# Optimization experiments

Measured on AMD Instinct MI355X. Metric: run time of the kernel, lower is better.

The kernel has to match this reference:

```python
import jax, jax.numpy as jnp
import numpy as np

N, E, SEQ, IN, HID, OUT = 2048, 65536, 5, 32, 64, 16
EPS = 1e-5


def setup_inputs() -> dict:
    ks = jax.random.split(jax.random.key(0), 16)
    def w(k, shape):
        return jax.random.normal(k, shape, jnp.float32) / np.float32(np.sqrt(shape[0]))
    z = lambda n: jnp.zeros((n,), jnp.float32)
    return dict(
        x=jax.random.normal(ks[0], (SEQ, N, IN), jnp.float32),
        edge_weight=jax.random.uniform(ks[1], (E,), jnp.float32),
        Wcz=w(ks[2], (IN, HID)), bcz=z(HID), Wlz=w(ks[3], (2 * HID, HID)), blz=z(HID),
        Wcr=w(ks[4], (IN, HID)), bcr=z(HID), Wlr=w(ks[5], (2 * HID, HID)), blr=z(HID),
        Wch=w(ks[6], (IN, HID)), bch=z(HID), Wlh=w(ks[7], (2 * HID, HID)), blh=z(HID),
        Wred=w(ks[8], (SEQ * HID, HID)), bred=z(HID),
        Wc1=w(ks[9], (HID, HID)), bc1=z(HID), Wc2=w(ks[10], (HID, HID)), bc2=z(HID),
        g1=jnp.ones((HID,), jnp.float32), be1=z(HID),
        g2=jnp.ones((HID,), jnp.float32), be2=z(HID),
        Wout=w(ks[11], (HID, OUT)), bout=z(OUT),
        Wi1=w(ks[12], (2 * HID, HID)), bi1=z(HID),
        Wi2=w(ks[13], (HID, 1)), bi2=z(1),
        edge_index=jax.random.randint(ks[14], (2, E), 0, N),
    )


def _layer_norm(h, g, b):
    mu = jnp.mean(h, -1, keepdims=True)
    var = jnp.mean((h - mu) ** 2, -1, keepdims=True)
    return (h - mu) * jax.lax.rsqrt(var + EPS) * g + b


def _forward(x, edge_weight, Wcz, bcz, Wlz, blz, Wcr, bcr, Wlr, blr,
             Wch, bch, Wlh, blh, Wred, bred, Wc1, bc1, Wc2, bc2,
             g1, be1, g2, be2, Wout, bout, Wi1, bi1, Wi2, bi2, edge_index):
    src, dst = edge_index[0], edge_index[1]
    # GCN symmetric normalization with self-loops (weight 1.0); shared by all convs.
    deg = jax.ops.segment_sum(edge_weight, dst, num_segments=N) + 1.0
    dinv = jax.lax.rsqrt(deg)
    norm = dinv[src] * edge_weight * dinv[dst]  # [E]
    dself = dinv * dinv                          # [N] self-loop coefficient

    def gcn(h, W, b):
        hw = h @ W
        agg = jax.ops.segment_sum(norm[:, None] * hw[src], dst, num_segments=N)
        return agg + dself[:, None] * hw + b

    # TGCN per timestep. The original passes no hidden state, so H resets to 0
    # each call: H_t = (1 - Z) * tanh(candidate); reset gate R is multiplied by
    # H=0 and has no effect (its params get zero gradient, matching torch).
    hs = []
    for t in range(SEQ):  # SEQ=5, fixed small loop
        Zg = jax.nn.sigmoid(gcn(x[t], Wcz, bcz) @ Wlz[:HID] + blz)
        Ht = jnp.tanh(gcn(x[t], Wch, bch) @ Wlh[:HID] + blh)
        hs.append((1.0 - Zg) * Ht)
    h = jnp.stack(hs, axis=1).reshape(N, SEQ * HID)
    h = h @ Wred + bred
    emb = h  # intermediate embeddings for the interaction predictor
    h = gcn(h, Wc1, bc1)
    h = jax.nn.relu(_layer_norm(h, g1, be1))  # dropout = identity in eval
    h = gcn(h, Wc2, bc2)
    h = jax.nn.relu(_layer_norm(h, g2, be2))
    node_pred = h @ Wout + bout
    # InteractionPredictor: cat([e_i, e_j]) @ Wi1 == e_i @ Wi1[:H] + e_j @ Wi1[H:]
    a = emb @ Wi1[:HID]
    bj = emb @ Wi1[HID:]
    hp = jax.nn.relu(a[:, None, :] + bj[None, :, :] + bi1)  # [N, N, HID]
    scores = (hp @ Wi2)[..., 0] + bi2[0]                     # [N, N]
    return node_pred, scores


def reference(x, edge_index, edge_weight, Wcz, bcz, Wlz, blz, Wcr, bcr, Wlr, blr,
              Wch, bch, Wlh, blh, Wred, bred, Wc1, bc1, Wc2, bc2,
              g1, be1, g2, be2, Wout, bout, Wi1, bi1, Wi2, bi2):
    return _forward(x, edge_weight, Wcz, bcz, Wlz, blz, Wcr, bcr, Wlr, blr,
                    Wch, bch, Wlh, blh, Wred, bred, Wc1, bc1, Wc2, bc2,
                    g1, be1, g2, be2, Wout, bout, Wi1, bi1, Wi2, bi2, edge_index)
```

## Files before the change

kernel.cpp:

```cpp
#include <hip/hip_runtime.h>
#include <math.h>

#define N_NODES 2048
#define N_EDGES 65536
#define SEQL 5
#define IN_F 32
#define HID 64
#define OUT_F 16
#define LN_EPS 1e-5f

__global__ __launch_bounds__(256) void k_deg_wcomb(
        const int* __restrict__ ei, const float* __restrict__ ew,
        const float* __restrict__ Wcz, const float* __restrict__ Wlz,
        const float* __restrict__ bcz, const float* __restrict__ blz,
        const float* __restrict__ Wch, const float* __restrict__ Wlh,
        const float* __restrict__ bch, const float* __restrict__ blh,
        float* __restrict__ deg, int* __restrict__ cnt,
        float* __restrict__ Wzp, float* __restrict__ Whp, float* __restrict__ bUV){
    int b = blockIdx.x, t = threadIdx.x;
    if (b < 256){
        int e = b * 256 + t;
        int d = ei[N_EDGES + e];
        atomicAdd(&deg[d], ew[e]);
        atomicAdd(&cnt[d], 1);
    } else {
        const float* Wc = (b == 256) ? Wcz : Wch;
        const float* Wl = (b == 256) ? Wlz : Wlh;
        const float* bc = (b == 256) ? bcz : bch;
        const float* bl = (b == 256) ? blz : blh;
        float* Wp = (b == 256) ? Wzp : Whp;
        for (int idx = t; idx < IN_F*HID; idx += 256){
            int i = idx >> 6, f = idx & 63;
            float s = 0.f;
            #pragma unroll 8
            for (int k = 0; k < HID; ++k) s += Wc[i*HID+k] * Wl[k*HID+f];
            Wp[idx] = s;
        }
        if (t < HID){
            float s = bl[t];
            for (int k = 0; k < HID; ++k) s += bc[k] * Wl[k*HID+t];
            bUV[(b-256)*HID + t] = s;
        }
    }
}

__global__ __launch_bounds__(1024) void k_scan(
        const float* __restrict__ deg, const int* __restrict__ cnt,
        int* __restrict__ rowptr, float* __restrict__ dinv, float* __restrict__ dself,
        int* __restrict__ fill){
    __shared__ int sc[1024];
    int t = threadIdx.x;
    int c0 = cnt[2*t], c1 = cnt[2*t+1];
    int ts = c0 + c1;
    sc[t] = ts;
    __syncthreads();
    for (int off = 1; off < 1024; off <<= 1){
        int v = (t >= off) ? sc[t - off] : 0;
        __syncthreads();
        sc[t] += v;
        __syncthreads();
    }
    int exc = sc[t] - ts;
    rowptr[2*t]   = exc;
    rowptr[2*t+1] = exc + c0;
    if (t == 1023) rowptr[N_NODES] = sc[t];
    float i0 = 1.f / sqrtf(deg[2*t] + 1.f);
    float i1 = 1.f / sqrtf(deg[2*t+1] + 1.f);
    dinv[2*t] = i0;     dinv[2*t+1] = i1;
    dself[2*t] = i0*i0; dself[2*t+1] = i1*i1;
    fill[2*t] = 0;      fill[2*t+1] = 0;
}

__global__ void k_csr(const int* __restrict__ ei, const float* __restrict__ ew,
                      const float* __restrict__ dinv, const int* __restrict__ rowptr,
                      int* __restrict__ fill, float2* __restrict__ cedge){
    int e = blockIdx.x * 256 + threadIdx.x;
    if (e < N_EDGES){
        int s = ei[e], d = ei[N_EDGES + e];
        int pos = rowptr[d] + atomicAdd(&fill[d], 1);
        float2 v;
        v.x = __int_as_float(s);
        v.y = dinv[s] * ew[e] * dinv[d];
        cedge[pos] = v;
    }
}

__global__ __launch_bounds__(320) void k_gate(const float* __restrict__ x,
        const float* __restrict__ dself, const int* __restrict__ rowptr,
        const float2* __restrict__ cedge,
        const float* __restrict__ bUV, const float* __restrict__ Wzp, const float* __restrict__ Whp,
        const float* __restrict__ Wred, const float* __restrict__ bred,
        const float* __restrict__ Wi1, const float* __restrict__ bi1, const float* __restrict__ Wc1,
        float* __restrict__ ag, float* __restrict__ bjp, float* __restrict__ hw1){
    int n = blockIdx.x;
    int tid = threadIdx.x;
    __shared__ float part[40*SEQL*IN_F];
    __shared__ float axs[SEQL][IN_F];
    __shared__ float hs[SEQL][HID];
    __shared__ float pw[SEQL][HID];
    __shared__ float hemb[HID];
    const int slot = tid >> 3, fl = tid & 7;
    const int f = tid & 63, t = tid >> 6;
    int beg = rowptr[n], end = rowptr[n+1];
    const float4* X4 = (const float4*)x;
    float4 a0 = {0,0,0,0}, a1 = {0,0,0,0}, a2 = {0,0,0,0}, a3 = {0,0,0,0}, a4 = {0,0,0,0};
    for (int p = beg + slot; p < end; p += 40){
        float2 ed = cedge[p];
        int s = __float_as_int(ed.x); float c = ed.y;
        float4 x0 = X4[(0*N_NODES + s)*8 + fl];
        float4 x1 = X4[(1*N_NODES + s)*8 + fl];
        float4 x2 = X4[(2*N_NODES + s)*8 + fl];
        float4 x3 = X4[(3*N_NODES + s)*8 + fl];
        float4 x4v= X4[(4*N_NODES + s)*8 + fl];
        a0.x += c*x0.x; a0.y += c*x0.y; a0.z += c*x0.z; a0.w += c*x0.w;
        a1.x += c*x1.x; a1.y += c*x1.y; a1.z += c*x1.z; a1.w += c*x1.w;
        a2.x += c*x2.x; a2.y += c*x2.y; a2.z += c*x2.z; a2.w += c*x2.w;
        a3.x += c*x3.x; a3.y += c*x3.y; a3.z += c*x3.z; a3.w += c*x3.w;
        a4.x += c*x4v.x; a4.y += c*x4v.y; a4.z += c*x4v.z; a4.w += c*x4v.w;
    }
    *(float4*)&part[(slot*SEQL + 0)*IN_F + fl*4] = a0;
    *(float4*)&part[(slot*SEQL + 1)*IN_F + fl*4] = a1;
    *(float4*)&part[(slot*SEQL + 2)*IN_F + fl*4] = a2;
    *(float4*)&part[(slot*SEQL + 3)*IN_F + fl*4] = a3;
    *(float4*)&part[(slot*SEQL + 4)*IN_F + fl*4] = a4;
    __syncthreads();
    if (tid < SEQL*IN_F){
        int tt = tid >> 5, ff = tid & 31;
        float s = dself[n] * x[(tt*N_NODES + n)*IN_F + ff];
        #pragma unroll 8
        for (int sl = 0; sl < 40; ++sl) s += part[(sl*SEQL + tt)*IN_F + ff];
        axs[tt][ff] = s;
    }
    __syncthreads();
    {
        float zz = bUV[f], hh = bUV[HID + f];
        #pragma unroll
        for (int i = 0; i < IN_F; ++i){
            float a = axs[t][i];
            zz += a * Wzp[i*HID + f];
            hh += a * Whp[i*HID + f];
        }
        float z = 1.f / (1.f + expf(-zz));
        hs[t][f] = (1.f - z) * tanhf(hh);
    }
    __syncthreads();
    {   float pp = 0.f;
        #pragma unroll
        for (int k = 0; k < HID; ++k) pp += hs[t][k] * Wred[(t*HID + k)*HID + f];
        pw[t][f] = pp;
    }
    __syncthreads();
    if (tid < HID){
        float hr = bred[tid];
        #pragma unroll
        for (int t2 = 0; t2 < SEQL; ++t2) hr += pw[t2][tid];
        hemb[tid] = hr;
    }
    __syncthreads();
    if (t < 3){
        const float* W = (t == 0) ? Wi1 : (t == 1) ? (Wi1 + HID*HID) : Wc1;
        float acc = (t == 1) ? bi1[f] : 0.f;
        #pragma unroll
        for (int k = 0; k < HID; ++k) acc += hemb[k] * W[k*HID + f];
        float* O = (t == 0) ? ag : (t == 1) ? bjp : hw1;
        O[n*HID + f] = acc;
    }
}

__global__ __launch_bounds__(512) void k_gcn1(
        const float* __restrict__ hw1, const float* __restrict__ dself,
        const int* __restrict__ rowptr, const float2* __restrict__ cedge,
        const float* __restrict__ bc1, const float* __restrict__ g1, const float* __restrict__ be1,
        const float* __restrict__ Wc2, float* __restrict__ hw2){
    int n = blockIdx.x;
    int tid = threadIdx.x;
    __shared__ float part[32*HID];
    __shared__ float hsh[HID];
    __shared__ float red8[8*HID];
    const int slot = tid >> 4, fl = tid & 15;
    const int f = tid & 63, w = tid >> 6;
    int beg = rowptr[n], end = rowptr[n+1];
    const float4* H4 = (const float4*)hw1;
    float4 acc = {0,0,0,0};
    for (int p = beg + slot; p < end; p += 32){
        float2 ed = cedge[p];
        int s = __float_as_int(ed.x); float c = ed.y;
        float4 h = H4[s*16 + fl];
        acc.x += c*h.x; acc.y += c*h.y; acc.z += c*h.z; acc.w += c*h.w;
    }
    *(float4*)&part[slot*HID + fl*4] = acc;
    __syncthreads();
    if (w == 0){
        float g = bc1[f] + dself[n] * hw1[n*HID + f];
        #pragma unroll 8
        for (int sl = 0; sl < 32; ++sl) g += part[sl*HID + f];
        float sum = g;
        for (int o = 32; o > 0; o >>= 1) sum += __shfl_xor(sum, o, 64);
        float mu = sum * (1.f/64.f);
        float d = g - mu;
        float vs = d * d;
        for (int o = 32; o > 0; o >>= 1) vs += __shfl_xor(vs, o, 64);
        float var = vs * (1.f/64.f);
        float h = d * (1.f / sqrtf(var + LN_EPS)) * g1[f] + be1[f];
        hsh[f] = fmaxf(h, 0.f);
    }
    __syncthreads();
    float s = 0.f;
    #pragma unroll
    for (int k = 0; k < 8; ++k) s += hsh[w*8 + k] * Wc2[(w*8 + k)*HID + f];
    red8[w*HID + f] = s;
    __syncthreads();
    if (w == 0){
        float o = 0.f;
        #pragma unroll
        for (int k = 0; k < 8; ++k) o += red8[k*HID + f];
        hw2[n*HID + f] = o;
    }
}

__global__ __launch_bounds__(512) void k_gcn2(
        const float* __restrict__ hw2, const float* __restrict__ dself,
        const int* __restrict__ rowptr, const float2* __restrict__ cedge,
        const float* __restrict__ bc2, const float* __restrict__ g2, const float* __restrict__ be2,
        const float* __restrict__ Wout, const float* __restrict__ bout, float* __restrict__ outp){
    int n = blockIdx.x;
    int tid = threadIdx.x;
    __shared__ float part[32*HID];
    __shared__ float hsh[HID];
    const int slot = tid >> 4, fl = tid & 15;
    const int f = tid & 63, w = tid >> 6;
    int beg = rowptr[n], end = rowptr[n+1];
    const float4* H4 = (const float4*)hw2;
    float4 acc = {0,0,0,0};
    for (int p = beg + slot; p < end; p += 32){
        float2 ed = cedge[p];
        int s = __float_as_int(ed.x); float c = ed.y;
        float4 h = H4[s*16 + fl];
        acc.x += c*h.x; acc.y += c*h.y; acc.z += c*h.z; acc.w += c*h.w;
    }
    *(float4*)&part[slot*HID + fl*4] = acc;
    __syncthreads();
    if (w == 0){
        float g = bc2[f] + dself[n] * hw2[n*HID + f];
        #pragma unroll 8
        for (int sl = 0; sl < 32; ++sl) g += part[sl*HID + f];
        float sum = g;
        for (int o = 32; o > 0; o >>= 1) sum += __shfl_xor(sum, o, 64);
        float mu = sum * (1.f/64.f);
        float d = g - mu;
        float vs = d * d;
        for (int o = 32; o > 0; o >>= 1) vs += __shfl_xor(vs, o, 64);
        float var = vs * (1.f/64.f);
        float h = d * (1.f / sqrtf(var + LN_EPS)) * g2[f] + be2[f];
        hsh[f] = fmaxf(h, 0.f);
    }
    __syncthreads();
    if (w == 0 && f < OUT_F){
        float s = bout[f];
        #pragma unroll
        for (int k = 0; k < HID; ++k) s += hsh[k] * Wout[k*OUT_F + f];
        outp[n*OUT_F + f] = s;
    }
}

__global__ __launch_bounds__(512) void k_scores(const float* __restrict__ ag, const float* __restrict__ bjp,
        const float* __restrict__ Wi2, const float* __restrict__ bi2, float* __restrict__ outs){
    __shared__ float as[128*36];
    __shared__ float bs[128*36];
    __shared__ float wv[64];
    int tid = threadIdx.x;
    int i0 = (blockIdx.x >> 4) * 128;
    int j0 = (blockIdx.x & 15) * 128;
    const float4* A4 = (const float4*)ag;
    const float4* B4 = (const float4*)bjp;
    if (tid < 64) wv[tid] = Wi2[tid];
    const int tj = tid & 15;
    const int rg = tid >> 4;
    float acc[4][8];
    #pragma unroll
    for (int k = 0; k < 4; ++k)
        #pragma unroll
        for (int m = 0; m < 8; ++m) acc[k][m] = 0.f;
    #pragma unroll
    for (int half = 0; half < 2; ++half){
        __syncthreads();
        #pragma unroll
        for (int k = 0; k < 2; ++k){
            int idx = tid + k*512;
            int r = idx >> 3, c = idx & 7;
            *(float4*)&as[r*36 + c*4] = A4[(i0 + r)*16 + half*8 + c];
            *(float4*)&bs[r*36 + c*4] = B4[(j0 + r)*16 + half*8 + c];
        }
        __syncthreads();
        #pragma unroll
        for (int fc = 0; fc < 8; ++fc){
            float4 w4 = *(float4*)&wv[half*32 + fc*4];
            float4 bv[8];
            #pragma unroll
            for (int m = 0; m < 8; ++m) bv[m] = *(float4*)&bs[(tj + 16*m)*36 + fc*4];
            #pragma unroll
            for (int k = 0; k < 4; ++k){
                float4 av = *(float4*)&as[(rg + 32*k)*36 + fc*4];
                #pragma unroll
                for (int m = 0; m < 8; ++m){
                    acc[k][m] = fmaf(fmaxf(av.x + bv[m].x, 0.f), w4.x, acc[k][m]);
                    acc[k][m] = fmaf(fmaxf(av.y + bv[m].y, 0.f), w4.y, acc[k][m]);
                    acc[k][m] = fmaf(fmaxf(av.z + bv[m].z, 0.f), w4.z, acc[k][m]);
                    acc[k][m] = fmaf(fmaxf(av.w + bv[m].w, 0.f), w4.w, acc[k][m]);
                }
            }
        }
    }
    float bi2v = bi2[0];
    #pragma unroll
    for (int k = 0; k < 4; ++k){
        #pragma unroll
        for (int m = 0; m < 8; ++m){
            long ro = (long)(i0 + rg + 32*k) * N_NODES + j0 + tj + 16*m;
            outs[ro] = acc[k][m] + bi2v;
        }
    }
}

extern "C" void kernel_launch(void* const* d_in, const int* in_sizes, int n_in,
                              void* d_out, int out_size, void* d_ws, size_t ws_size,
                              hipStream_t stream){
    const float* x   = (const float*)d_in[0];
    const float* ew  = (const float*)d_in[1];
    const float* Wcz = (const float*)d_in[2];  const float* bcz = (const float*)d_in[3];
    const float* Wlz = (const float*)d_in[4];  const float* blz = (const float*)d_in[5];
    const float* Wch = (const float*)d_in[10]; const float* bch = (const float*)d_in[11];
    const float* Wlh = (const float*)d_in[12]; const float* blh = (const float*)d_in[13];
    const float* Wred= (const float*)d_in[14]; const float* bred= (const float*)d_in[15];
    const float* Wc1 = (const float*)d_in[16]; const float* bc1 = (const float*)d_in[17];
    const float* Wc2 = (const float*)d_in[18]; const float* bc2 = (const float*)d_in[19];
    const float* g1  = (const float*)d_in[20]; const float* be1 = (const float*)d_in[21];
    const float* g2  = (const float*)d_in[22]; const float* be2 = (const float*)d_in[23];
    const float* Wout= (const float*)d_in[24]; const float* bout= (const float*)d_in[25];
    const float* Wi1 = (const float*)d_in[26]; const float* bi1 = (const float*)d_in[27];
    const float* Wi2 = (const float*)d_in[28]; const float* bi2 = (const float*)d_in[29];
    const int*  ei  = (const int*)d_in[30];

    float* w = (float*)d_ws;
    float* deg    = w;
    int*   cnt    = (int*)(w + 2048);
    int*   rowptr = (int*)(w + 4096);
    float* dinv   = w + 6656;
    float* dself  = w + 8704;
    int*   fill   = (int*)(w + 10752);
    float2* cedge = (float2*)(w + 12800);
    float* Wzp    = w + 143872;
    float* Whp    = w + 145920;
    float* bUV    = w + 147968;
    float* ag     = w + 148096;
    float* bjp    = w + 279168;
    float* hw1    = w + 410240;
    float* hw2    = w + 541312;

    hipMemsetAsync(deg, 0, 16384, stream);
    k_deg_wcomb<<<258, 256, 0, stream>>>(ei, ew, Wcz, Wlz, bcz, blz, Wch, Wlh, bch, blh,
                                         deg, cnt, Wzp, Whp, bUV);
    k_scan<<<1, 1024, 0, stream>>>(deg, cnt, rowptr, dinv, dself, fill);
    k_csr<<<N_EDGES/256, 256, 0, stream>>>(ei, ew, dinv, rowptr, fill, cedge);
    k_gate<<<N_NODES, 320, 0, stream>>>(x, dself, rowptr, cedge, bUV, Wzp, Whp,
                                        Wred, bred, Wi1, bi1, Wc1, ag, bjp, hw1);
    k_gcn1<<<N_NODES, 512, 0, stream>>>(hw1, dself, rowptr, cedge, bc1, g1, be1, Wc2, hw2);
    k_gcn2<<<N_NODES, 512, 0, stream>>>(hw2, dself, rowptr, cedge, bc2, g2, be2, Wout, bout,
                                        (float*)d_out);
    k_scores<<<256, 512, 0, stream>>>(ag, bjp, Wi2, bi2, (float*)d_out + N_NODES*OUT_F);
}
```

Baseline: 218.3 us.

## Merge pairwise score kernel into GCN1 launch as extra blocks

The score-tile kernel becomes an extra 256 blocks appended to the first GCN aggregation launch, with both paths sharing one union of shared memory. Both depend only on outputs of k_gate, so the compute-heavy score tiles can fill the GPU alongside the memory-bound gather blocks, and one launch is removed. The costs are that the merged kernel allocates the larger shared footprint (about 37 KB) for every block, which may lower occupancy of the GCN blocks, and that register pressure follows the score path.

```diff
diff --git a/kernel.cpp b/kernel.cpp
--- a/kernel.cpp
+++ b/kernel.cpp
@@ -167,54 +167,117 @@
     }
 }
 
-__global__ __launch_bounds__(512) void k_gcn1(
+__global__ __launch_bounds__(512) void k_gcn1s(
         const float* __restrict__ hw1, const float* __restrict__ dself,
         const int* __restrict__ rowptr, const float2* __restrict__ cedge,
         const float* __restrict__ bc1, const float* __restrict__ g1, const float* __restrict__ be1,
-        const float* __restrict__ Wc2, float* __restrict__ hw2){
-    int n = blockIdx.x;
+        const float* __restrict__ Wc2, float* __restrict__ hw2,
+        const float* __restrict__ ag, const float* __restrict__ bjp,
+        const float* __restrict__ Wi2, const float* __restrict__ bi2,
+        float* __restrict__ outs){
+    __shared__ float LP[9280];
+    int blk = blockIdx.x;
     int tid = threadIdx.x;
-    __shared__ float part[32*HID];
-    __shared__ float hsh[HID];
-    __shared__ float red8[8*HID];
-    const int slot = tid >> 4, fl = tid & 15;
-    const int f = tid & 63, w = tid >> 6;
-    int beg = rowptr[n], end = rowptr[n+1];
-    const float4* H4 = (const float4*)hw1;
-    float4 acc = {0,0,0,0};
-    for (int p = beg + slot; p < end; p += 32){
-        float2 ed = cedge[p];
-        int s = __float_as_int(ed.x); float c = ed.y;
-        float4 h = H4[s*16 + fl];
-        acc.x += c*h.x; acc.y += c*h.y; acc.z += c*h.z; acc.w += c*h.w;
-    }
-    *(float4*)&part[slot*HID + fl*4] = acc;
-    __syncthreads();
-    if (w == 0){
-        float g = bc1[f] + dself[n] * hw1[n*HID + f];
-        #pragma unroll 8
-        for (int sl = 0; sl < 32; ++sl) g += part[sl*HID + f];
-        float sum = g;
-        for (int o = 32; o > 0; o >>= 1) sum += __shfl_xor(sum, o, 64);
-        float mu = sum * (1.f/64.f);
-        float d = g - mu;
-        float vs = d * d;
-        for (int o = 32; o > 0; o >>= 1) vs += __shfl_xor(vs, o, 64);
-        float var = vs * (1.f/64.f);
-        float h = d * (1.f / sqrtf(var + LN_EPS)) * g1[f] + be1[f];
-        hsh[f] = fmaxf(h, 0.f);
-    }
-    __syncthreads();
-    float s = 0.f;
-    #pragma unroll
-    for (int k = 0; k < 8; ++k) s += hsh[w*8 + k] * Wc2[(w*8 + k)*HID + f];
-    red8[w*HID + f] = s;
-    __syncthreads();
-    if (w == 0){
-        float o = 0.f;
-        #pragma unroll
-        for (int k = 0; k < 8; ++k) o += red8[k*HID + f];
-        hw2[n*HID + f] = o;
+    if (blk < N_NODES){
+        float* part = LP;
+        float* hsh  = LP + 2048;
+        float* red8 = LP + 2112;
+        int n = blk;
+        const int slot = tid >> 4, fl = tid & 15;
+        const int f = tid & 63, w = tid >> 6;
+        int beg = rowptr[n], end = rowptr[n+1];
+        const float4* H4 = (const float4*)hw1;
+        float4 acc = {0,0,0,0};
+        for (int p = beg + slot; p < end; p += 32){
+            float2 ed = cedge[p];
+            int s = __float_as_int(ed.x); float c = ed.y;
+            float4 h = H4[s*16 + fl];
+            acc.x += c*h.x; acc.y += c*h.y; acc.z += c*h.z; acc.w += c*h.w;
+        }
+        *(float4*)&part[slot*HID + fl*4] = acc;
+        __syncthreads();
+        if (w == 0){
+            float g = bc1[f] + dself[n] * hw1[n*HID + f];
+            #pragma unroll 8
+            for (int sl = 0; sl < 32; ++sl) g += part[sl*HID + f];
+            float sum = g;
+            for (int o = 32; o > 0; o >>= 1) sum += __shfl_xor(sum, o, 64);
+            float mu = sum * (1.f/64.f);
+            float d = g - mu;
+            float vs = d * d;
+            for (int o = 32; o > 0; o >>= 1) vs += __shfl_xor(vs, o, 64);
+            float var = vs * (1.f/64.f);
+            float h = d * (1.f / sqrtf(var + LN_EPS)) * g1[f] + be1[f];
+            hsh[f] = fmaxf(h, 0.f);
+        }
+        __syncthreads();
+        float s = 0.f;
+        #pragma unroll
+        for (int k = 0; k < 8; ++k) s += hsh[w*8 + k] * Wc2[(w*8 + k)*HID + f];
+        red8[w*HID + f] = s;
+        __syncthreads();
+        if (w == 0){
+            float o = 0.f;
+            #pragma unroll
+            for (int k = 0; k < 8; ++k) o += red8[k*HID + f];
+            hw2[n*HID + f] = o;
+        }
+    } else {
+        float* as = LP;
+        float* bs = LP + 4608;
+        float* wv = LP + 9216;
+        int tl = blk - N_NODES;
+        int i0 = (tl >> 4) * 128;
+        int j0 = (tl & 15) * 128;
+        const float4* A4 = (const float4*)ag;
+        const float4* B4 = (const float4*)bjp;
+        if (tid < 64) wv[tid] = Wi2[tid];
+        const int tj = tid & 15;
+        const int rg = tid >> 4;
+        float acc[4][8];
+        #pragma unroll
+        for (int k = 0; k < 4; ++k)
+            #pragma unroll
+            for (int m = 0; m < 8; ++m) acc[k][m] = 0.f;
+        #pragma unroll
+        for (int half = 0; half < 2; ++half){
+            __syncthreads();
+            #pragma unroll
+            for (int k = 0; k < 2; ++k){
+                int idx = tid + k*512;
+                int r = idx >> 3, c = idx & 7;
+                *(float4*)&as[r*36 + c*4] = A4[(i0 + r)*16 + half*8 + c];
+                *(float4*)&bs[r*36 + c*4] = B4[(j0 + r)*16 + half*8 + c];
+            }
+            __syncthreads();
+            #pragma unroll
+            for (int fc = 0; fc < 8; ++fc){
+                float4 w4 = *(float4*)&wv[half*32 + fc*4];
+                float4 bv[8];
+                #pragma unroll
+                for (int m = 0; m < 8; ++m) bv[m] = *(float4*)&bs[(tj + 16*m)*36 + fc*4];
+                #pragma unroll
+                for (int k = 0; k < 4; ++k){
+                    float4 av = *(float4*)&as[(rg + 32*k)*36 + fc*4];
+                    #pragma unroll
+                    for (int m = 0; m < 8; ++m){
+                        acc[k][m] = fmaf(fmaxf(av.x + bv[m].x, 0.f), w4.x, acc[k][m]);
+                        acc[k][m] = fmaf(fmaxf(av.y + bv[m].y, 0.f), w4.y, acc[k][m]);
+                        acc[k][m] = fmaf(fmaxf(av.z + bv[m].z, 0.f), w4.z, acc[k][m]);
+                        acc[k][m] = fmaf(fmaxf(av.w + bv[m].w, 0.f), w4.w, acc[k][m]);
+                    }
+                }
+            }
+        }
+        float bi2v = bi2[0];
+        #pragma unroll
+        for (int k = 0; k < 4; ++k){
+            #pragma unroll
+            for (int m = 0; m < 8; ++m){
+                long ro = (long)(i0 + rg + 32*k) * N_NODES + j0 + tj + 16*m;
+                outs[ro] = acc[k][m] + bi2v;
+            }
+        }
     }
 }
 
@@ -263,65 +326,6 @@
     }
 }
 
-__global__ __launch_bounds__(512) void k_scores(const float* __restrict__ ag, const float* __restrict__ bjp,
-        const float* __restrict__ Wi2, const float* __restrict__ bi2, float* __restrict__ outs){
-    __shared__ float as[128*36];
-    __shared__ float bs[128*36];
-    __shared__ float wv[64];
-    int tid = threadIdx.x;
-    int i0 = (blockIdx.x >> 4) * 128;
-    int j0 = (blockIdx.x & 15) * 128;
-    const float4* A4 = (const float4*)ag;
-    const float4* B4 = (const float4*)bjp;
-    if (tid < 64) wv[tid] = Wi2[tid];
-    const int tj = tid & 15;
-    const int rg = tid >> 4;
-    float acc[4][8];
-    #pragma unroll
-    for (int k = 0; k < 4; ++k)
-        #pragma unroll
-        for (int m = 0; m < 8; ++m) acc[k][m] = 0.f;
-    #pragma unroll
-    for (int half = 0; half < 2; ++half){
-        __syncthreads();
-        #pragma unroll
-        for (int k = 0; k < 2; ++k){
-            int idx = tid + k*512;
-            int r = idx >> 3, c = idx & 7;
-            *(float4*)&as[r*36 + c*4] = A4[(i0 + r)*16 + half*8 + c];
-            *(float4*)&bs[r*36 + c*4] = B4[(j0 + r)*16 + half*8 + c];
-        }
-        __syncthreads();
-        #pragma unroll
-        for (int fc = 0; fc < 8; ++fc){
-            float4 w4 = *(float4*)&wv[half*32 + fc*4];
-            float4 bv[8];
-            #pragma unroll
-            for (int m = 0; m < 8; ++m) bv[m] = *(float4*)&bs[(tj + 16*m)*36 + fc*4];
-            #pragma unroll
-            for (int k = 0; k < 4; ++k){
-                float4 av = *(float4*)&as[(rg + 32*k)*36 + fc*4];
-                #pragma unroll
-                for (int m = 0; m < 8; ++m){
-                    acc[k][m] = fmaf(fmaxf(av.x + bv[m].x, 0.f), w4.x, acc[k][m]);
-                    acc[k][m] = fmaf(fmaxf(av.y + bv[m].y, 0.f), w4.y, acc[k][m]);
-                    acc[k][m] = fmaf(fmaxf(av.z + bv[m].z, 0.f), w4.z, acc[k][m]);
-                    acc[k][m] = fmaf(fmaxf(av.w + bv[m].w, 0.f), w4.w, acc[k][m]);
-                }
-            }
-        }
-    }
-    float bi2v = bi2[0];
-    #pragma unroll
-    for (int k = 0; k < 4; ++k){
-        #pragma unroll
-        for (int m = 0; m < 8; ++m){
-            long ro = (long)(i0 + rg + 32*k) * N_NODES + j0 + tj + 16*m;
-            outs[ro] = acc[k][m] + bi2v;
-        }
-    }
-}
-
 extern "C" void kernel_launch(void* const* d_in, const int* in_sizes, int n_in,
                               void* d_out, int out_size, void* d_ws, size_t ws_size,
                               hipStream_t stream){
@@ -364,8 +368,9 @@
     k_csr<<<N_EDGES/256, 256, 0, stream>>>(ei, ew, dinv, rowptr, fill, cedge);
     k_gate<<<N_NODES, 320, 0, stream>>>(x, dself, rowptr, cedge, bUV, Wzp, Whp,
                                         Wred, bred, Wi1, bi1, Wc1, ag, bjp, hw1);
-    k_gcn1<<<N_NODES, 512, 0, stream>>>(hw1, dself, rowptr, cedge, bc1, g1, be1, Wc2, hw2);
+    k_gcn1s<<<N_NODES + 256, 512, 0, stream>>>(hw1, dself, rowptr, cedge, bc1, g1, be1, Wc2, hw2,
+                                               ag, bjp, Wi2, bi2,
+                                               (float*)d_out + N_NODES*OUT_F);
     k_gcn2<<<N_NODES, 512, 0, stream>>>(hw2, dself, rowptr, cedge, bc2, g2, be2, Wout, bout,
                                         (float*)d_out);
-    k_scores<<<256, 512, 0, stream>>>(ag, bjp, Wi2, bi2, (float*)d_out + N_NODES*OUT_F);
-}
+}
```

Result: slower. 231.4 us (+6.0%).
